# Optimization experiments

Hardware: AMD Instinct MI355X
Metric: run time of the kernel (lower is better)

## Reference

```python
import jax, jax.numpy as jnp
import numpy as np
import math

CHANNEL = 512
NUM_HEAD = 8
HEAD_DIM = 64


def setup_inputs() -> dict:
    key = jax.random.key(0)
    ks = jax.random.split(key, 9)
    d = NUM_HEAD * HEAD_DIM  # 512
    s = 1.0 / math.sqrt(CHANNEL)
    return {
        "x": jax.random.normal(ks[0], (8, CHANNEL, 32, 32), dtype=jnp.float32),
        "wq": jax.random.normal(ks[1], (CHANNEL, d), dtype=jnp.float32) * s,
        "bq": jnp.zeros((d,), dtype=jnp.float32),
        "wk": jax.random.normal(ks[2], (CHANNEL, d), dtype=jnp.float32) * s,
        "bk": jnp.zeros((d,), dtype=jnp.float32),
        "wv": jax.random.normal(ks[3], (CHANNEL, d), dtype=jnp.float32) * s,
        "bv": jnp.zeros((d,), dtype=jnp.float32),
        "wo": jax.random.normal(ks[4], (d, CHANNEL), dtype=jnp.float32) * s,
        "bo": jnp.zeros((CHANNEL,), dtype=jnp.float32),
    }


def reference(x, wq, bq, wk, bk, wv, bv, wo, bo):
    B, C, H, W = x.shape
    S = H * W
    # [B, C, H, W] -> [B, S, C]
    xr = x.transpose(0, 2, 3, 1).reshape(B, S, C)
    q = (xr @ wq + bq).reshape(B, S, NUM_HEAD, HEAD_DIM)
    k = (xr @ wk + bk).reshape(B, S, NUM_HEAD, HEAD_DIM)
    v = (xr @ wv + bv).reshape(B, S, NUM_HEAD, HEAD_DIM)
    # NOTE: original scales by 1/sqrt(channel), not 1/sqrt(head_dim)
    energy = jnp.einsum('bqhd,bkhd->bhqk', q, k) / math.sqrt(C)
    attn = jax.nn.softmax(energy, axis=-1)
    out = jnp.einsum('bhqk,bkhd->bqhd', attn, v).reshape(B, S, NUM_HEAD * HEAD_DIM)
    out = out @ wo + bo  # [B, S, C]
    out = out.transpose(0, 2, 1).reshape(B, C, H, W)
    return x + out
```

## Files before the change

### kernel.cpp

```cpp
#include <hip/hip_runtime.h>
#include <hip/hip_bf16.h>

typedef __bf16 bf16_t;
typedef __attribute__((ext_vector_type(8))) __bf16 bf16x8;
typedef __attribute__((ext_vector_type(4))) __bf16 bf16x4;
typedef __attribute__((ext_vector_type(4))) float f32x4;

#define AS1 __attribute__((address_space(1)))
#define AS3 __attribute__((address_space(3)))

__device__ __forceinline__ void gload_lds16(const void* g, void* l) {
  __builtin_amdgcn_global_load_lds((const AS1 void*)g, (AS3 void*)l, 16, 0, 0);
}

__global__ void __launch_bounds__(256) prep_kernel(
    const float* __restrict__ x, const float* __restrict__ w0,
    const float* __restrict__ w1, const float* __restrict__ w2,
    const float* __restrict__ w3, bf16_t* __restrict__ xr, bf16_t* __restrict__ t0,
    bf16_t* __restrict__ t1, bf16_t* __restrict__ t2, bf16_t* __restrict__ t3) {
  __shared__ float tile[64][69];
  int t = blockIdx.x;
  const float* src;
  bf16_t* dst;
  int ld_src, ld_dst, R0, C0;
  if (t < 256) {
    int z = t >> 6, rem = t & 63;
    src = (z == 0) ? w0 : (z == 1) ? w1 : (z == 2) ? w2 : w3;
    dst = (z == 0) ? t0 : (z == 1) ? t1 : (z == 2) ? t2 : t3;
    ld_src = 512; ld_dst = 512;
    R0 = (rem >> 3) * 64;
    C0 = (rem & 7) * 64;
  } else {
    t -= 256;
    int b = t >> 7, rem = t & 127;
    src = x + (size_t)b * 512 * 1024;
    dst = xr + (size_t)b * 1024 * 512;
    ld_src = 1024; ld_dst = 512;
    R0 = (rem >> 4) * 64;
    C0 = (rem & 15) * 64;
  }
  const int tid = threadIdx.x;
  const int rl = tid >> 4;
  const int cl = (tid & 15) * 4;
#pragma unroll
  for (int p = 0; p < 4; ++p) {
    int r = p * 16 + rl;
    float4 v = *(const float4*)(src + (size_t)(R0 + r) * ld_src + C0 + cl);
    tile[r][cl + 0] = v.x;
    tile[r][cl + 1] = v.y;
    tile[r][cl + 2] = v.z;
    tile[r][cl + 3] = v.w;
  }
  __syncthreads();
  const int kk = tid & 7;
  const int cw = tid >> 3;
#pragma unroll
  for (int p = 0; p < 2; ++p) {
    int c = p * 32 + cw;
    bf16x8 o;
#pragma unroll
    for (int j = 0; j < 8; ++j) o[j] = (bf16_t)tile[kk * 8 + j][c];
    *(bf16x8*)(dst + (size_t)(C0 + c) * ld_dst + R0 + kk * 8) = o;
  }
}

__device__ __forceinline__ void gemm_nt_128x128_p4(const bf16_t* __restrict__ Abase,
                                                   const bf16_t* __restrict__ Bbase,
                                                   bf16_t (*As)[128 * 32],
                                                   bf16_t (*Bs)[128 * 32],
                                                   f32x4 acc[4][4]) {
  const int tid = threadIdx.x;
  const int lane = tid & 63;
  const int wid = tid >> 6;
  const int wr = wid >> 1, wc = wid & 1;
  const int lrow = lane & 15;
  const int kgrp = lane >> 4;
  const int r0 = tid >> 2;
  const int cb = (tid & 3) * 16;

#pragma unroll
  for (int p = 0; p < 2; ++p) {
    const int kt = p * 32;
#pragma unroll
    for (int j = 0; j < 2; ++j) {
      int row = j * 64 + r0;
      gload_lds16((const char*)(Abase + row * 512 + kt) + cb, (char*)As[p] + row * 64 + cb);
    }
#pragma unroll
    for (int j = 0; j < 2; ++j) {
      int row = j * 64 + r0;
      gload_lds16((const char*)(Bbase + row * 512 + kt) + cb, (char*)Bs[p] + row * 64 + cb);
    }
  }

  for (int t = 0; t < 16; ++t) {
    const int cur = t & 3;
    if (t < 14) {
      const int nxt = (t + 2) & 3;
      const int kt = (t + 2) * 32;
#pragma unroll
      for (int j = 0; j < 2; ++j) {
        int row = j * 64 + r0;
        gload_lds16((const char*)(Abase + row * 512 + kt) + cb,
                    (char*)As[nxt] + row * 64 + cb);
      }
#pragma unroll
      for (int j = 0; j < 2; ++j) {
        int row = j * 64 + r0;
        gload_lds16((const char*)(Bbase + row * 512 + kt) + cb,
                    (char*)Bs[nxt] + row * 64 + cb);
      }
      asm volatile("s_waitcnt vmcnt(8)" ::: "memory");
    } else if (t == 14) {
      asm volatile("s_waitcnt vmcnt(4)" ::: "memory");
    } else {
      asm volatile("s_waitcnt vmcnt(0)" ::: "memory");
    }
    __builtin_amdgcn_sched_barrier(0);
    __builtin_amdgcn_s_barrier();

    bf16x8 a[4], b[4];
#pragma unroll
    for (int mf = 0; mf < 4; ++mf)
      a[mf] = *(const bf16x8*)(As[cur] + (wr * 64 + mf * 16 + lrow) * 32 + kgrp * 8);
#pragma unroll
    for (int nf = 0; nf < 4; ++nf)
      b[nf] = *(const bf16x8*)(Bs[cur] + (wc * 64 + nf * 16 + lrow) * 32 + kgrp * 8);
    __builtin_amdgcn_s_setprio(1);
#pragma unroll
    for (int mf = 0; mf < 4; ++mf)
#pragma unroll
      for (int nf = 0; nf < 4; ++nf)
        acc[mf][nf] = __builtin_amdgcn_mfma_f32_16x16x32_bf16(a[mf], b[nf], acc[mf][nf], 0, 0, 0);
    __builtin_amdgcn_s_setprio(0);
  }
}

__device__ __forceinline__ void gemm_nt_128x256_p3(const bf16_t* __restrict__ Abase,
                                                   const bf16_t* __restrict__ Bbase,
                                                   bf16_t (*As)[128 * 32],
                                                   bf16_t (*Bs)[256 * 32],
                                                   f32x4 acc[4][8]) {
  const int tid = threadIdx.x;
  const int lane = tid & 63;
  const int wid = tid >> 6;
  const int wr = wid >> 1, wc = wid & 1;
  const int lrow = lane & 15;
  const int kgrp = lane >> 4;
  const int r0 = tid >> 2;
  const int cb = (tid & 3) * 16;

#pragma unroll
  for (int p = 0; p < 2; ++p) {
    const int kt = p * 32;
#pragma unroll
    for (int j = 0; j < 2; ++j) {
      int row = j * 64 + r0;
      gload_lds16((const char*)(Abase + row * 512 + kt) + cb, (char*)As[p] + row * 64 + cb);
    }
#pragma unroll
    for (int j = 0; j < 4; ++j) {
      int row = j * 64 + r0;
      gload_lds16((const char*)(Bbase + row * 512 + kt) + cb, (char*)Bs[p] + row * 64 + cb);
    }
  }
  asm volatile("s_waitcnt vmcnt(6)" ::: "memory");
  __builtin_amdgcn_sched_barrier(0);

  int cur = 0, nxt = 2;
  for (int t = 0; t < 16; ++t) {
    __builtin_amdgcn_s_barrier();
    __builtin_amdgcn_sched_barrier(0);
    if (t < 14) {
      const int kt = (t + 2) * 32;
#pragma unroll
      for (int j = 0; j < 2; ++j) {
        int row = j * 64 + r0;
        gload_lds16((const char*)(Abase + row * 512 + kt) + cb,
                    (char*)As[nxt] + row * 64 + cb);
      }
#pragma unroll
      for (int j = 0; j < 4; ++j) {
        int row = j * 64 + r0;
        gload_lds16((const char*)(Bbase + row * 512 + kt) + cb,
                    (char*)Bs[nxt] + row * 64 + cb);
      }
    }

    bf16x8 a[4], b[8];
#pragma unroll
    for (int mf = 0; mf < 4; ++mf)
      a[mf] = *(const bf16x8*)(As[cur] + (wr * 64 + mf * 16 + lrow) * 32 + kgrp * 8);
#pragma unroll
    for (int nf = 0; nf < 8; ++nf)
      b[nf] = *(const bf16x8*)(Bs[cur] + (wc * 128 + nf * 16 + lrow) * 32 + kgrp * 8);
    __builtin_amdgcn_s_setprio(1);
#pragma unroll
    for (int mf = 0; mf < 4; ++mf)
#pragma unroll
      for (int nf = 0; nf < 8; ++nf)
        acc[mf][nf] = __builtin_amdgcn_mfma_f32_16x16x32_bf16(a[mf], b[nf], acc[mf][nf], 0, 0, 0);
    __builtin_amdgcn_s_setprio(0);
    if (t < 14) {
      asm volatile("s_waitcnt vmcnt(6)" ::: "memory");
    } else {
      asm volatile("s_waitcnt vmcnt(0)" ::: "memory");
    }
    __builtin_amdgcn_sched_barrier(0);
    cur = (cur == 2) ? 0 : cur + 1;
    nxt = (nxt == 2) ? 0 : nxt + 1;
  }
}

__global__ void __launch_bounds__(256, 2) gemm_qkv_kernel(
    const bf16_t* __restrict__ xr, const bf16_t* __restrict__ wT ,
    const float* __restrict__ bq, const float* __restrict__ bk,
    const float* __restrict__ bv, bf16_t* __restrict__ qo, bf16_t* __restrict__ ko,
    bf16_t* __restrict__ vto) {
  __shared__ bf16_t As[3][128 * 32];
  __shared__ bf16_t Bs[3][256 * 32];
  const int bn = blockIdx.x, bm = blockIdx.y;
  const int z = bn >> 1;
  const float* bias = (z == 0) ? bq : (z == 1) ? bk : bv;
  f32x4 acc[4][8] = {};
  gemm_nt_128x256_p3(xr + bm * 128 * 512, wT + (size_t)bn * 256 * 512, As, Bs, acc);
  const int lane = threadIdx.x & 63, wid = threadIdx.x >> 6;
  const int lrow = lane & 15, kgrp = lane >> 4;
  const int wr = wid >> 1, wc = wid & 1;
  const int row0 = bm * 128 + wr * 64;
  const int col0 = bn * 256 + wc * 128;
  const float qscale = 0.044194173824159216f * 1.4426950408889634f;
  if (z == 2) {
#pragma unroll
    for (int mf = 0; mf < 4; ++mf)
#pragma unroll
      for (int nf = 0; nf < 8; ++nf) {
        int nl = (col0 + nf * 16 + lrow) & 511;
        int h = nl >> 6, d = nl & 63;
        float bb = bias[nl];
        int m0 = row0 + mf * 16 + kgrp * 4;
        int b = m0 >> 10, s = m0 & 1023;
        bf16x4 pk;
#pragma unroll
        for (int r = 0; r < 4; ++r) pk[r] = (bf16_t)(acc[mf][nf][r] + bb);
        *(bf16x4*)(vto + (((size_t)(b * 8 + h) * 64 + d) * 1024 + s)) = pk;
      }
  } else {
    bf16_t* out = (z == 0) ? qo : ko;
    const float sc = (z == 0) ? qscale : 1.0f;
#pragma unroll
    for (int mf = 0; mf < 4; ++mf)
#pragma unroll
      for (int nf = 0; nf < 8; ++nf) {
        int nl = (col0 + nf * 16 + lrow) & 511;
        int h = nl >> 6, d = nl & 63;
        float bb = bias[nl];
#pragma unroll
        for (int r = 0; r < 4; ++r) {
          int m = row0 + mf * 16 + kgrp * 4 + r;
          int b = m >> 10, s = m & 1023;
          out[((b * 8 + h) * 1024 + s) * 64 + d] = (bf16_t)((acc[mf][nf][r] + bb) * sc);
        }
      }
  }
}

__global__ void __launch_bounds__(256, 2) attn_kernel(const bf16_t* __restrict__ q,
                                                      const bf16_t* __restrict__ k,
                                                      const bf16_t* __restrict__ vt,
                                                      bf16_t* __restrict__ attn_out) {
  __shared__ char Ks[4][8192];
  __shared__ char Vs[4][8192];
  __shared__ char Ps[4][4096];
  const int tid = threadIdx.x;
  const int lane = tid & 63, wid = tid >> 6;
  const int lrow = lane & 15, kgrp = lane >> 4;
  const int bh = blockIdx.x, qb = blockIdx.y;
  const int b = bh >> 3, h = bh & 7;

  const char* khb = (const char*)(k + (size_t)bh * 1024 * 64);
  const char* vthb = (const char*)(vt + (size_t)bh * 64 * 1024);
  const bf16_t* qh = q + (size_t)bh * 1024 * 64;

  const int qbase = qb * 128 + wid * 32;
  bf16x8 qa[2][2];
#pragma unroll
  for (int qf = 0; qf < 2; ++qf) {
    int qrow = qbase + qf * 16 + lrow;
    qa[qf][0] = *(const bf16x8*)(qh + qrow * 64 + kgrp * 8);
    qa[qf][1] = *(const bf16x8*)(qh + qrow * 64 + 32 + kgrp * 8);
  }

  char* Pw = Ps[wid];
  const int srow = tid >> 3;
  const int sc2 = tid & 7;

  float l_part[2] = {0.f, 0.f};
  f32x4 o[2][4] = {};

#pragma unroll
  for (int p = 0; p < 2; ++p) {
    const char* kg = khb + p * (64 * 128);
    const char* vg = vthb + p * 128;
#pragma unroll
    for (int j = 0; j < 2; ++j) {
      int row = j * 32 + srow;
      gload_lds16(kg + row * 128 + ((sc2 ^ (row & 7)) * 16), Ks[p] + j * 4096 + tid * 16);
    }
#pragma unroll
    for (int j = 0; j < 2; ++j) {
      int row = j * 32 + srow;
      gload_lds16(vg + row * 2048 + ((sc2 ^ (row & 7)) * 16), Vs[p] + j * 4096 + tid * 16);
    }
  }

  for (int t = 0; t < 16; ++t) {
    const int cur = t & 3;
    if (t < 14) {
      const int nxt = (t + 2) & 3;
      const char* kg = khb + (t + 2) * (64 * 128);
      const char* vg = vthb + (t + 2) * 128;
#pragma unroll
      for (int j = 0; j < 2; ++j) {
        int row = j * 32 + srow;
        gload_lds16(kg + row * 128 + ((sc2 ^ (row & 7)) * 16),
                    Ks[nxt] + j * 4096 + tid * 16);
      }
#pragma unroll
      for (int j = 0; j < 2; ++j) {
        int row = j * 32 + srow;
        gload_lds16(vg + row * 2048 + ((sc2 ^ (row & 7)) * 16),
                    Vs[nxt] + j * 4096 + tid * 16);
      }
      asm volatile("s_waitcnt vmcnt(8)" ::: "memory");
    } else if (t == 14) {
      asm volatile("s_waitcnt vmcnt(4)" ::: "memory");
    } else {
      asm volatile("s_waitcnt vmcnt(0)" ::: "memory");
    }
    __builtin_amdgcn_sched_barrier(0);
    __builtin_amdgcn_s_barrier();

    const char* Kc = Ks[cur];
    const char* Vc = Vs[cur];

    f32x4 sa[2][4] = {};
    __builtin_amdgcn_s_setprio(1);
#pragma unroll
    for (int c = 0; c < 4; ++c) {
      int krow = c * 16 + lrow;
      bf16x8 k0 = *(const bf16x8*)(Kc + krow * 128 + ((kgrp ^ (krow & 7)) * 16));
      bf16x8 k1 = *(const bf16x8*)(Kc + krow * 128 + (((4 + kgrp) ^ (krow & 7)) * 16));
#pragma unroll
      for (int qf = 0; qf < 2; ++qf) {
        sa[qf][c] = __builtin_amdgcn_mfma_f32_16x16x32_bf16(k0, qa[qf][0], sa[qf][c], 0, 0, 0);
        sa[qf][c] = __builtin_amdgcn_mfma_f32_16x16x32_bf16(k1, qa[qf][1], sa[qf][c], 0, 0, 0);
      }
    }
    __builtin_amdgcn_s_setprio(0);

#pragma unroll
    for (int qf = 0; qf < 2; ++qf) {
      int prow = qf * 16 + lrow;
      float rs = 0.f;
#pragma unroll
      for (int c = 0; c < 4; ++c) {
        bf16x4 pk;
#pragma unroll
        for (int r = 0; r < 4; ++r) {
          float p = exp2f(sa[qf][c][r]);
          rs += p;
          pk[r] = (bf16_t)p;
        }
        int chunk = (c * 2 + (kgrp >> 1)) ^ (prow & 7);
        *(bf16x4*)(Pw + prow * 128 + chunk * 16 + (kgrp & 1) * 8) = pk;
      }
      l_part[qf] += rs;
    }

    __builtin_amdgcn_s_setprio(1);
#pragma unroll
    for (int kk = 0; kk < 2; ++kk) {
      bf16x8 pa[2];
#pragma unroll
      for (int qf = 0; qf < 2; ++qf) {
        int prow = qf * 16 + lrow;
        int pchunk = (kk * 4 + kgrp) ^ (prow & 7);
        pa[qf] = *(const bf16x8*)(Pw + prow * 128 + pchunk * 16);
      }
#pragma unroll
      for (int nfo = 0; nfo < 4; ++nfo) {
        int vrow = nfo * 16 + lrow;
        int vchunk = (kk * 4 + kgrp) ^ (vrow & 7);
        bf16x8 vb = *(const bf16x8*)(Vc + vrow * 128 + vchunk * 16);
#pragma unroll
        for (int qf = 0; qf < 2; ++qf)
          o[qf][nfo] = __builtin_amdgcn_mfma_f32_16x16x32_bf16(pa[qf], vb, o[qf][nfo], 0, 0, 0);
      }
    }
    __builtin_amdgcn_s_setprio(0);
  }

#pragma unroll
  for (int qf = 0; qf < 2; ++qf) {
    l_part[qf] += __shfl_xor(l_part[qf], 16, 64);
    l_part[qf] += __shfl_xor(l_part[qf], 32, 64);
  }
#pragma unroll
  for (int qf = 0; qf < 2; ++qf)
#pragma unroll
    for (int r = 0; r < 4; ++r) {
      float inv = 1.0f / __shfl(l_part[qf], kgrp * 4 + r, 64);
      int s = qbase + qf * 16 + kgrp * 4 + r;
#pragma unroll
      for (int nfo = 0; nfo < 4; ++nfo) {
        int d = nfo * 16 + lrow;
        attn_out[((b * 1024 + s) * 8 + h) * 64 + d] = (bf16_t)(o[qf][nfo][r] * inv);
      }
    }
}

__global__ void __launch_bounds__(256, 2) gemm_out_kernel(const bf16_t* __restrict__ woT,
                                                          const bf16_t* __restrict__ attn,
                                                          const float* __restrict__ x,
                                                          const float* __restrict__ bo,
                                                          float* __restrict__ out) {
  __shared__ bf16_t As[4][128 * 32];
  __shared__ bf16_t Bs[4][128 * 32];
  const int bn = blockIdx.x, bm = blockIdx.y;
  f32x4 acc[4][4] = {};
  gemm_nt_128x128_p4(woT + bm * 128 * 512, attn + bn * 128 * 512, As, Bs, acc);
  const int lane = threadIdx.x & 63, wid = threadIdx.x >> 6;
  const int wr = wid >> 1, wc = wid & 1;
  const int c0 = bm * 128 + wr * 64;
  const int s0g = bn * 128 + wc * 64;
#pragma unroll
  for (int mf = 0; mf < 4; ++mf)
#pragma unroll
    for (int r = 0; r < 4; ++r) {
      int c = c0 + mf * 16 + (lane >> 4) * 4 + r;
      float bias = bo[c];
#pragma unroll
      for (int nf = 0; nf < 4; ++nf) {
        int n = s0g + nf * 16 + (lane & 15);
        int b = n >> 10, s = n & 1023;
        int idx = (b * 512 + c) * 1024 + s;
        out[idx] = x[idx] + acc[mf][nf][r] + bias;
      }
    }
}

extern "C" void kernel_launch(void* const* d_in, const int* in_sizes, int n_in,
                              void* d_out, int out_size, void* d_ws, size_t ws_size,
                              hipStream_t stream) {
  const float* x  = (const float*)d_in[0];
  const float* wq = (const float*)d_in[1];
  const float* bq = (const float*)d_in[2];
  const float* wk = (const float*)d_in[3];
  const float* bk = (const float*)d_in[4];
  const float* wv = (const float*)d_in[5];
  const float* bv = (const float*)d_in[6];
  const float* wo = (const float*)d_in[7];
  const float* bo = (const float*)d_in[8];
  float* out = (float*)d_out;

  char* ws = (char*)d_ws;
  const size_t SZ_XR = (size_t)8192 * 512 * 2;
  const size_t SZ_W  = (size_t)512 * 512 * 2;
  const size_t SZ_T  = (size_t)8 * 8 * 1024 * 64 * 2;
  bf16_t* xr   = (bf16_t*)(ws);
  bf16_t* wqT  = (bf16_t*)(ws + SZ_XR);
  bf16_t* wkT  = (bf16_t*)(ws + SZ_XR + SZ_W);
  bf16_t* wvT  = (bf16_t*)(ws + SZ_XR + 2 * SZ_W);
  bf16_t* woT  = (bf16_t*)(ws + SZ_XR + 3 * SZ_W);
  bf16_t* qd   = (bf16_t*)(ws + SZ_XR + 4 * SZ_W);
  bf16_t* kd   = (bf16_t*)(ws + SZ_XR + 4 * SZ_W + SZ_T);
  bf16_t* vtd  = (bf16_t*)(ws + SZ_XR + 4 * SZ_W + 2 * SZ_T);
  bf16_t* attn = (bf16_t*)(ws);

  prep_kernel<<<dim3(1280), 256, 0, stream>>>(x, wq, wk, wv, wo, xr, wqT, wkT, wvT, woT);
  gemm_qkv_kernel<<<dim3(6, 64), 256, 0, stream>>>(xr, wqT, bq, bk, bv, qd, kd, vtd);
  attn_kernel<<<dim3(64, 8), 256, 0, stream>>>(qd, kd, vtd, attn);
  gemm_out_kernel<<<dim3(64, 4), 256, 0, stream>>>(woT, attn, x, bo, out);
}
```

Before: 84.41 us.

## Halve barriers in attention loop and shrink output GEMM tile to 64x128

The attention kernel's KV loop now processes two 64-key tiles per iteration. Each iteration issues prefetch loads for two future tiles and synchronizes once instead of per tile, halving barrier and waitcnt overhead. The output projection GEMM moves from 128x128 to 64x128 tiles, doubling its grid from 256 to 512 blocks to fill more CUs on the device. The smaller tile lowers per-block arithmetic intensity, and the coarser attention prefetch changes load/compute overlap.

```diff
diff --git a/kernel.cpp b/kernel.cpp
--- a/kernel.cpp
+++ b/kernel.cpp
@@ -64,78 +64,6 @@
   }
 }
 
-__device__ __forceinline__ void gemm_nt_128x128_p4(const bf16_t* __restrict__ Abase,
-                                                   const bf16_t* __restrict__ Bbase,
-                                                   bf16_t (*As)[128 * 32],
-                                                   bf16_t (*Bs)[128 * 32],
-                                                   f32x4 acc[4][4]) {
-  const int tid = threadIdx.x;
-  const int lane = tid & 63;
-  const int wid = tid >> 6;
-  const int wr = wid >> 1, wc = wid & 1;
-  const int lrow = lane & 15;
-  const int kgrp = lane >> 4;
-  const int r0 = tid >> 2;
-  const int cb = (tid & 3) * 16;
-
-#pragma unroll
-  for (int p = 0; p < 2; ++p) {
-    const int kt = p * 32;
-#pragma unroll
-    for (int j = 0; j < 2; ++j) {
-      int row = j * 64 + r0;
-      gload_lds16((const char*)(Abase + row * 512 + kt) + cb, (char*)As[p] + row * 64 + cb);
-    }
-#pragma unroll
-    for (int j = 0; j < 2; ++j) {
-      int row = j * 64 + r0;
-      gload_lds16((const char*)(Bbase + row * 512 + kt) + cb, (char*)Bs[p] + row * 64 + cb);
-    }
-  }
-
-  for (int t = 0; t < 16; ++t) {
-    const int cur = t & 3;
-    if (t < 14) {
-      const int nxt = (t + 2) & 3;
-      const int kt = (t + 2) * 32;
-#pragma unroll
-      for (int j = 0; j < 2; ++j) {
-        int row = j * 64 + r0;
-        gload_lds16((const char*)(Abase + row * 512 + kt) + cb,
-                    (char*)As[nxt] + row * 64 + cb);
-      }
-#pragma unroll
-      for (int j = 0; j < 2; ++j) {
-        int row = j * 64 + r0;
-        gload_lds16((const char*)(Bbase + row * 512 + kt) + cb,
-                    (char*)Bs[nxt] + row * 64 + cb);
-      }
-      asm volatile("s_waitcnt vmcnt(8)" ::: "memory");
-    } else if (t == 14) {
-      asm volatile("s_waitcnt vmcnt(4)" ::: "memory");
-    } else {
-      asm volatile("s_waitcnt vmcnt(0)" ::: "memory");
-    }
-    __builtin_amdgcn_sched_barrier(0);
-    __builtin_amdgcn_s_barrier();
-
-    bf16x8 a[4], b[4];
-#pragma unroll
-    for (int mf = 0; mf < 4; ++mf)
-      a[mf] = *(const bf16x8*)(As[cur] + (wr * 64 + mf * 16 + lrow) * 32 + kgrp * 8);
-#pragma unroll
-    for (int nf = 0; nf < 4; ++nf)
-      b[nf] = *(const bf16x8*)(Bs[cur] + (wc * 64 + nf * 16 + lrow) * 32 + kgrp * 8);
-    __builtin_amdgcn_s_setprio(1);
-#pragma unroll
-    for (int mf = 0; mf < 4; ++mf)
-#pragma unroll
-      for (int nf = 0; nf < 4; ++nf)
-        acc[mf][nf] = __builtin_amdgcn_mfma_f32_16x16x32_bf16(a[mf], b[nf], acc[mf][nf], 0, 0, 0);
-    __builtin_amdgcn_s_setprio(0);
-  }
-}
-
 __device__ __forceinline__ void gemm_nt_128x256_p3(const bf16_t* __restrict__ Abase,
                                                    const bf16_t* __restrict__ Bbase,
                                                    bf16_t (*As)[128 * 32],
@@ -300,7 +228,7 @@
 
 #pragma unroll
   for (int p = 0; p < 2; ++p) {
-    const char* kg = khb + p * (64 * 128);
+    const char* kg = khb + p * 8192;
     const char* vg = vthb + p * 128;
 #pragma unroll
     for (int j = 0; j < 2; ++j) {
@@ -314,91 +242,97 @@
     }
   }
 
-  for (int t = 0; t < 16; ++t) {
-    const int cur = t & 3;
-    if (t < 14) {
-      const int nxt = (t + 2) & 3;
-      const char* kg = khb + (t + 2) * (64 * 128);
-      const char* vg = vthb + (t + 2) * 128;
-#pragma unroll
-      for (int j = 0; j < 2; ++j) {
-        int row = j * 32 + srow;
-        gload_lds16(kg + row * 128 + ((sc2 ^ (row & 7)) * 16),
-                    Ks[nxt] + j * 4096 + tid * 16);
-      }
-#pragma unroll
-      for (int j = 0; j < 2; ++j) {
-        int row = j * 32 + srow;
-        gload_lds16(vg + row * 2048 + ((sc2 ^ (row & 7)) * 16),
-                    Vs[nxt] + j * 4096 + tid * 16);
+  for (int T = 0; T < 8; ++T) {
+    __builtin_amdgcn_s_barrier();
+    __builtin_amdgcn_sched_barrier(0);
+    if (T < 7) {
+#pragma unroll
+      for (int p = 0; p < 2; ++p) {
+        const int u = 2 * T + 2 + p;
+        const int bu = u & 3;
+        const char* kg = khb + u * 8192;
+        const char* vg = vthb + u * 128;
+#pragma unroll
+        for (int j = 0; j < 2; ++j) {
+          int row = j * 32 + srow;
+          gload_lds16(kg + row * 128 + ((sc2 ^ (row & 7)) * 16),
+                      Ks[bu] + j * 4096 + tid * 16);
+        }
+#pragma unroll
+        for (int j = 0; j < 2; ++j) {
+          int row = j * 32 + srow;
+          gload_lds16(vg + row * 2048 + ((sc2 ^ (row & 7)) * 16),
+                      Vs[bu] + j * 4096 + tid * 16);
+        }
       }
       asm volatile("s_waitcnt vmcnt(8)" ::: "memory");
-    } else if (t == 14) {
-      asm volatile("s_waitcnt vmcnt(4)" ::: "memory");
     } else {
       asm volatile("s_waitcnt vmcnt(0)" ::: "memory");
     }
     __builtin_amdgcn_sched_barrier(0);
-    __builtin_amdgcn_s_barrier();
-
-    const char* Kc = Ks[cur];
-    const char* Vc = Vs[cur];
-
-    f32x4 sa[2][4] = {};
-    __builtin_amdgcn_s_setprio(1);
-#pragma unroll
-    for (int c = 0; c < 4; ++c) {
-      int krow = c * 16 + lrow;
-      bf16x8 k0 = *(const bf16x8*)(Kc + krow * 128 + ((kgrp ^ (krow & 7)) * 16));
-      bf16x8 k1 = *(const bf16x8*)(Kc + krow * 128 + (((4 + kgrp) ^ (krow & 7)) * 16));
-#pragma unroll
-      for (int qf = 0; qf < 2; ++qf) {
-        sa[qf][c] = __builtin_amdgcn_mfma_f32_16x16x32_bf16(k0, qa[qf][0], sa[qf][c], 0, 0, 0);
-        sa[qf][c] = __builtin_amdgcn_mfma_f32_16x16x32_bf16(k1, qa[qf][1], sa[qf][c], 0, 0, 0);
-      }
-    }
-    __builtin_amdgcn_s_setprio(0);
-
-#pragma unroll
-    for (int qf = 0; qf < 2; ++qf) {
-      int prow = qf * 16 + lrow;
-      float rs = 0.f;
+
+#pragma unroll
+    for (int half = 0; half < 2; ++half) {
+      const int bu = (2 * T + half) & 3;
+      const char* Kc = Ks[bu];
+      const char* Vc = Vs[bu];
+
+      f32x4 sa[2][4] = {};
+      __builtin_amdgcn_s_setprio(1);
 #pragma unroll
       for (int c = 0; c < 4; ++c) {
-        bf16x4 pk;
-#pragma unroll
-        for (int r = 0; r < 4; ++r) {
-          float p = exp2f(sa[qf][c][r]);
-          rs += p;
-          pk[r] = (bf16_t)p;
-        }
-        int chunk = (c * 2 + (kgrp >> 1)) ^ (prow & 7);
-        *(bf16x4*)(Pw + prow * 128 + chunk * 16 + (kgrp & 1) * 8) = pk;
-      }
-      l_part[qf] += rs;
-    }
-
-    __builtin_amdgcn_s_setprio(1);
-#pragma unroll
-    for (int kk = 0; kk < 2; ++kk) {
-      bf16x8 pa[2];
+        int krow = c * 16 + lrow;
+        bf16x8 k0 = *(const bf16x8*)(Kc + krow * 128 + ((kgrp ^ (krow & 7)) * 16));
+        bf16x8 k1 = *(const bf16x8*)(Kc + krow * 128 + (((4 + kgrp) ^ (krow & 7)) * 16));
+#pragma unroll
+        for (int qf = 0; qf < 2; ++qf) {
+          sa[qf][c] = __builtin_amdgcn_mfma_f32_16x16x32_bf16(k0, qa[qf][0], sa[qf][c], 0, 0, 0);
+          sa[qf][c] = __builtin_amdgcn_mfma_f32_16x16x32_bf16(k1, qa[qf][1], sa[qf][c], 0, 0, 0);
+        }
+      }
+      __builtin_amdgcn_s_setprio(0);
+
 #pragma unroll
       for (int qf = 0; qf < 2; ++qf) {
         int prow = qf * 16 + lrow;
-        int pchunk = (kk * 4 + kgrp) ^ (prow & 7);
-        pa[qf] = *(const bf16x8*)(Pw + prow * 128 + pchunk * 16);
-      }
-#pragma unroll
-      for (int nfo = 0; nfo < 4; ++nfo) {
-        int vrow = nfo * 16 + lrow;
-        int vchunk = (kk * 4 + kgrp) ^ (vrow & 7);
-        bf16x8 vb = *(const bf16x8*)(Vc + vrow * 128 + vchunk * 16);
-#pragma unroll
-        for (int qf = 0; qf < 2; ++qf)
-          o[qf][nfo] = __builtin_amdgcn_mfma_f32_16x16x32_bf16(pa[qf], vb, o[qf][nfo], 0, 0, 0);
-      }
-    }
-    __builtin_amdgcn_s_setprio(0);
+        float rs = 0.f;
+#pragma unroll
+        for (int c = 0; c < 4; ++c) {
+          bf16x4 pk;
+#pragma unroll
+          for (int r = 0; r < 4; ++r) {
+            float p = exp2f(sa[qf][c][r]);
+            rs += p;
+            pk[r] = (bf16_t)p;
+          }
+          int chunk = (c * 2 + (kgrp >> 1)) ^ (prow & 7);
+          *(bf16x4*)(Pw + prow * 128 + chunk * 16 + (kgrp & 1) * 8) = pk;
+        }
+        l_part[qf] += rs;
+      }
+
+      __builtin_amdgcn_s_setprio(1);
+#pragma unroll
+      for (int kk = 0; kk < 2; ++kk) {
+        bf16x8 pa[2];
+#pragma unroll
+        for (int qf = 0; qf < 2; ++qf) {
+          int prow = qf * 16 + lrow;
+          int pchunk = (kk * 4 + kgrp) ^ (prow & 7);
+          pa[qf] = *(const bf16x8*)(Pw + prow * 128 + pchunk * 16);
+        }
+#pragma unroll
+        for (int nfo = 0; nfo < 4; ++nfo) {
+          int vrow = nfo * 16 + lrow;
+          int vchunk = (kk * 4 + kgrp) ^ (vrow & 7);
+          bf16x8 vb = *(const bf16x8*)(Vc + vrow * 128 + vchunk * 16);
+#pragma unroll
+          for (int qf = 0; qf < 2; ++qf)
+            o[qf][nfo] = __builtin_amdgcn_mfma_f32_16x16x32_bf16(pa[qf], vb, o[qf][nfo], 0, 0, 0);
+        }
+      }
+      __builtin_amdgcn_s_setprio(0);
+    }
   }
 
 #pragma unroll
@@ -425,24 +359,80 @@
                                                           const float* __restrict__ x,
                                                           const float* __restrict__ bo,
                                                           float* __restrict__ out) {
-  __shared__ bf16_t As[4][128 * 32];
+  __shared__ bf16_t As[4][64 * 32];
   __shared__ bf16_t Bs[4][128 * 32];
   const int bn = blockIdx.x, bm = blockIdx.y;
-  f32x4 acc[4][4] = {};
-  gemm_nt_128x128_p4(woT + bm * 128 * 512, attn + bn * 128 * 512, As, Bs, acc);
-  const int lane = threadIdx.x & 63, wid = threadIdx.x >> 6;
+  const bf16_t* Abase = woT + bm * 64 * 512;
+  const bf16_t* Bbase = attn + bn * 128 * 512;
+  const int tid = threadIdx.x;
+  const int lane = tid & 63;
+  const int wid = tid >> 6;
   const int wr = wid >> 1, wc = wid & 1;
-  const int c0 = bm * 128 + wr * 64;
+  const int lrow = lane & 15;
+  const int kgrp = lane >> 4;
+  const int r0 = tid >> 2;
+  const int cb = (tid & 3) * 16;
+  f32x4 acc[2][4] = {};
+
+#pragma unroll
+  for (int p = 0; p < 2; ++p) {
+    const int kt = p * 32;
+    gload_lds16((const char*)(Abase + r0 * 512 + kt) + cb, (char*)As[p] + r0 * 64 + cb);
+#pragma unroll
+    for (int j = 0; j < 2; ++j) {
+      int row = j * 64 + r0;
+      gload_lds16((const char*)(Bbase + row * 512 + kt) + cb, (char*)Bs[p] + row * 64 + cb);
+    }
+  }
+
+  for (int t = 0; t < 16; ++t) {
+    const int cur = t & 3;
+    if (t < 14) {
+      const int nxt = (t + 2) & 3;
+      const int kt = (t + 2) * 32;
+      gload_lds16((const char*)(Abase + r0 * 512 + kt) + cb, (char*)As[nxt] + r0 * 64 + cb);
+#pragma unroll
+      for (int j = 0; j < 2; ++j) {
+        int row = j * 64 + r0;
+        gload_lds16((const char*)(Bbase + row * 512 + kt) + cb,
+                    (char*)Bs[nxt] + row * 64 + cb);
+      }
+      asm volatile("s_waitcnt vmcnt(6)" ::: "memory");
+    } else if (t == 14) {
+      asm volatile("s_waitcnt vmcnt(3)" ::: "memory");
+    } else {
+      asm volatile("s_waitcnt vmcnt(0)" ::: "memory");
+    }
+    __builtin_amdgcn_sched_barrier(0);
+    __builtin_amdgcn_s_barrier();
+
+    bf16x8 a[2], bfr[4];
+#pragma unroll
+    for (int mf = 0; mf < 2; ++mf)
+      a[mf] = *(const bf16x8*)(As[cur] + (wr * 32 + mf * 16 + lrow) * 32 + kgrp * 8);
+#pragma unroll
+    for (int nf = 0; nf < 4; ++nf)
+      bfr[nf] = *(const bf16x8*)(Bs[cur] + (wc * 64 + nf * 16 + lrow) * 32 + kgrp * 8);
+    __builtin_amdgcn_s_setprio(1);
+#pragma unroll
+    for (int mf = 0; mf < 2; ++mf)
+#pragma unroll
+      for (int nf = 0; nf < 4; ++nf)
+        acc[mf][nf] = __builtin_amdgcn_mfma_f32_16x16x32_bf16(a[mf], bfr[nf], acc[mf][nf], 0, 0, 0);
+    __builtin_amdgcn_s_setprio(0);
+  }
+
+  const int c0 = bm * 64 + wr * 32;
   const int s0g = bn * 128 + wc * 64;
 #pragma unroll
-  for (int mf = 0; mf < 4; ++mf)
+  for (int mf = 0; mf < 2; ++mf)
 #pragma unroll
     for (int r = 0; r < 4; ++r) {
-      int c = c0 + mf * 16 + (lane >> 4) * 4 + r;
+      int c = c0 + mf * 16 + kgrp * 4 + r;
       float bias = bo[c];
 #pragma unroll
       for (int nf = 0; nf < 4; ++nf) {
-        int n = s0g + nf * 16 + (lane & 15);
+        int n = s0g + nf * 16 + lrow;
         int b = n >> 10, s = n & 1023;
         int idx = (b * 512 + c) * 1024 + s;
         out[idx] = x[idx] + acc[mf][nf][r] + bias;
@@ -481,5 +471,5 @@
   prep_kernel<<<dim3(1280), 256, 0, stream>>>(x, wq, wk, wv, wo, xr, wqT, wkT, wvT, woT);
   gemm_qkv_kernel<<<dim3(6, 64), 256, 0, stream>>>(xr, wqT, bq, bk, bv, qd, kd, vtd);
   attn_kernel<<<dim3(64, 8), 256, 0, stream>>>(qd, kd, vtd, attn);
-  gemm_out_kernel<<<dim3(64, 4), 256, 0, stream>>>(woT, attn, x, bo, out);
-}
+  gemm_out_kernel<<<dim3(64, 8), 256, 0, stream>>>(woT, attn, x, bo, out);
+}
```

New measurement: 81.89 us. 1.03x faster.
